# Performance work log

Measured on AMD Instinct MI355X. Metric: run time of the kernel, lower is better.

The kernel has to match this reference:

```python
import jax, jax.numpy as jnp
import numpy as np

N, C = 262144, 512
EPS = 1e-7


def setup_inputs() -> dict:
    key = jax.random.key(0)
    k1, k2, k3 = jax.random.split(key, 3)
    close_er = jax.random.normal(k1, (N, C), dtype=jnp.float32)
    y = jax.random.randint(k2, (N,), 0, C, dtype=jnp.int64)
    max_dis = jax.random.normal(k3, (C,), dtype=jnp.float32)
    margin = jnp.float32(0.5)
    return {"close_er": close_er, "y": y, "max_dis": max_dis, "margin": margin}


def reference(close_er, y, max_dis, margin):
    # Original: for each class i, take samples with y==i, compute
    # -log(clamp(sigmoid(close_er[idx, i] - max_dis[i] - margin))).mean(),
    # then average over classes that have at least one sample.
    num_classes = max_dis.shape[0]
    # Per-sample gather of its own-class distance: close_er[n, y[n]]
    ce = jnp.take_along_axis(close_er, y[:, None], axis=1)[:, 0]  # [N]
    md = max_dis[y]  # [N]
    gap = jax.nn.sigmoid(ce - md - margin)
    gap = jnp.clip(gap, EPS, 1.0 - EPS)
    nll = -jnp.log(gap)  # [N]
    # Per-class sum and count in one segment-reduce pass over N.
    sums = jax.ops.segment_sum(nll, y, num_segments=num_classes)  # [C]
    counts = jax.ops.segment_sum(jnp.ones_like(nll), y, num_segments=num_classes)  # [C]
    nonempty = counts > 0
    means = jnp.where(nonempty, sums / jnp.maximum(counts, 1.0), 0.0)
    j = jnp.sum(nonempty).astype(means.dtype)
    return jnp.sum(means) / j
```

## Files before the change

kernel.cpp:

```cpp
#include <hip/hip_runtime.h>

#define N_CLASSES 512
#define EPS_F 1e-7f

__global__ __launch_bounds__(1024) void nll_hist_kernel(
    const float* __restrict__ close_er,
    const int*   __restrict__ y,
    const float* __restrict__ max_dis,
    const float* __restrict__ margin_p,
    float* __restrict__ g_sums,
    float* __restrict__ g_counts,
    int n)
{
    __shared__ float        s_md[N_CLASSES];
    __shared__ float        s_sum[N_CLASSES];
    __shared__ unsigned int s_cnt[N_CLASSES];

    const int tid = threadIdx.x;
    const float margin = margin_p[0];

    for (int c = tid; c < N_CLASSES; c += blockDim.x) {
        s_md[c]  = max_dis[c];
        s_sum[c] = 0.0f;
        s_cnt[c] = 0u;
    }
    __syncthreads();

    for (long long i = (long long)blockIdx.x * blockDim.x + tid; i < n;
         i += (long long)gridDim.x * blockDim.x) {
        const int c = y[i];
        const float ce = close_er[i * (long long)N_CLASSES + c];
        const float x  = ce - s_md[c] - margin;
        float s = 1.0f / (1.0f + __expf(-x));
        s = fminf(fmaxf(s, EPS_F), 1.0f - EPS_F);
        const float nll = -__logf(s);
        atomicAdd(&s_sum[c], nll);
        atomicAdd(&s_cnt[c], 1u);
    }
    __syncthreads();

    for (int c = tid; c < N_CLASSES; c += blockDim.x) {
        const unsigned int cnt = s_cnt[c];
        if (cnt != 0u) {
            atomicAdd(&g_sums[c],   s_sum[c]);
            atomicAdd(&g_counts[c], (float)cnt);
        }
    }
}

__global__ __launch_bounds__(512) void finalize_kernel(
    const float* __restrict__ g_sums,
    const float* __restrict__ g_counts,
    float* __restrict__ out)
{
    __shared__ float s_m[N_CLASSES];
    __shared__ float s_j[N_CLASSES];

    const int t = threadIdx.x;
    const float cnt  = g_counts[t];
    const bool  ne   = cnt > 0.0f;
    s_m[t] = ne ? (g_sums[t] / cnt) : 0.0f;
    s_j[t] = ne ? 1.0f : 0.0f;
    __syncthreads();

    for (int off = 256; off >= 64; off >>= 1) {
        if (t < off) {
            s_m[t] += s_m[t + off];
            s_j[t] += s_j[t + off];
        }
        __syncthreads();
    }
    if (t < 64) {
        float m = s_m[t];
        float j = s_j[t];
        for (int off = 32; off > 0; off >>= 1) {
            m += __shfl_down(m, off);
            j += __shfl_down(j, off);
        }
        if (t == 0) out[0] = m / j;
    }
}

extern "C" void kernel_launch(void* const* d_in, const int* in_sizes, int n_in,
                              void* d_out, int out_size, void* d_ws, size_t ws_size,
                              hipStream_t stream) {
    const float* close_er = (const float*)d_in[0];
    const int*   y        = (const int*)d_in[1];
    const float* max_dis  = (const float*)d_in[2];
    const float* margin   = (const float*)d_in[3];
    float* out = (float*)d_out;

    const int n = in_sizes[1];

    float* g_sums   = (float*)d_ws;
    float* g_counts = g_sums + N_CLASSES;

    hipMemsetAsync(d_ws, 0, 2 * N_CLASSES * sizeof(float), stream);

    const int block = 1024;
    const int grid  = (n + block - 1) / block;
    nll_hist_kernel<<<grid, block, 0, stream>>>(close_er, y, max_dis, margin,
                                                g_sums, g_counts, n);
    finalize_kernel<<<1, N_CLASSES, 0, stream>>>(g_sums, g_counts, out);
}
```

Before: 21.70 us.

## Fuse finalize into histogram kernel via last-block ticket and batch four samples per thread

```diff
diff --git a/kernel.cpp b/kernel.cpp
--- a/kernel.cpp
+++ b/kernel.cpp
@@ -2,82 +2,122 @@
 
 #define N_CLASSES 512
 #define EPS_F 1e-7f
+#define BLOCK 256
+#define SPT 4
 
-__global__ __launch_bounds__(1024) void nll_hist_kernel(
+__global__ __launch_bounds__(BLOCK) void nll_fused_kernel(
     const float* __restrict__ close_er,
     const int*   __restrict__ y,
     const float* __restrict__ max_dis,
     const float* __restrict__ margin_p,
     float* __restrict__ g_sums,
     float* __restrict__ g_counts,
+    int*   __restrict__ g_ticket,
+    float* __restrict__ out,
     int n)
 {
     __shared__ float        s_md[N_CLASSES];
     __shared__ float        s_sum[N_CLASSES];
     __shared__ unsigned int s_cnt[N_CLASSES];
+    __shared__ float        s_red[8];
+    __shared__ bool         s_last;
 
     const int tid = threadIdx.x;
     const float margin = margin_p[0];
 
-    for (int c = tid; c < N_CLASSES; c += blockDim.x) {
+    for (int c = tid; c < N_CLASSES; c += BLOCK) {
         s_md[c]  = max_dis[c];
         s_sum[c] = 0.0f;
         s_cnt[c] = 0u;
     }
     __syncthreads();
 
-    for (long long i = (long long)blockIdx.x * blockDim.x + tid; i < n;
-         i += (long long)gridDim.x * blockDim.x) {
-        const int c = y[i];
-        const float ce = close_er[i * (long long)N_CLASSES + c];
-        const float x  = ce - s_md[c] - margin;
-        float s = 1.0f / (1.0f + __expf(-x));
-        s = fminf(fmaxf(s, EPS_F), 1.0f - EPS_F);
-        const float nll = -__logf(s);
-        atomicAdd(&s_sum[c], nll);
-        atomicAdd(&s_cnt[c], 1u);
+    const int base = (blockIdx.x * BLOCK + tid) * SPT;
+    if (base + SPT <= n) {
+        const int4 y4 = *reinterpret_cast<const int4*>(&y[base]);
+        const int c0 = y4.x, c1 = y4.y, c2 = y4.z, c3 = y4.w;
+        const float ce0 = close_er[(size_t)(base + 0) * N_CLASSES + c0];
+        const float ce1 = close_er[(size_t)(base + 1) * N_CLASSES + c1];
+        const float ce2 = close_er[(size_t)(base + 2) * N_CLASSES + c2];
+        const float ce3 = close_er[(size_t)(base + 3) * N_CLASSES + c3];
+        const float x0 = ce0 - s_md[c0] - margin;
+        const float x1 = ce1 - s_md[c1] - margin;
+        const float x2 = ce2 - s_md[c2] - margin;
+        const float x3 = ce3 - s_md[c3] - margin;
+        float s0 = 1.0f / (1.0f + __expf(-x0));
+        float s1 = 1.0f / (1.0f + __expf(-x1));
+        float s2 = 1.0f / (1.0f + __expf(-x2));
+        float s3 = 1.0f / (1.0f + __expf(-x3));
+        s0 = fminf(fmaxf(s0, EPS_F), 1.0f - EPS_F);
+        s1 = fminf(fmaxf(s1, EPS_F), 1.0f - EPS_F);
+        s2 = fminf(fmaxf(s2, EPS_F), 1.0f - EPS_F);
+        s3 = fminf(fmaxf(s3, EPS_F), 1.0f - EPS_F);
+        atomicAdd(&s_sum[c0], -__logf(s0));
+        atomicAdd(&s_sum[c1], -__logf(s1));
+        atomicAdd(&s_sum[c2], -__logf(s2));
+        atomicAdd(&s_sum[c3], -__logf(s3));
+        atomicAdd(&s_cnt[c0], 1u);
+        atomicAdd(&s_cnt[c1], 1u);
+        atomicAdd(&s_cnt[c2], 1u);
+        atomicAdd(&s_cnt[c3], 1u);
+    } else {
+        for (int k = 0; k < SPT; ++k) {
+            const int i = base + k;
+            if (i < n) {
+                const int c = y[i];
+                const float ce = close_er[(size_t)i * N_CLASSES + c];
+                const float x  = ce - s_md[c] - margin;
+                float s = 1.0f / (1.0f + __expf(-x));
+                s = fminf(fmaxf(s, EPS_F), 1.0f - EPS_F);
+                atomicAdd(&s_sum[c], -__logf(s));
+                atomicAdd(&s_cnt[c], 1u);
+            }
+        }
     }
     __syncthreads();
 
-    for (int c = tid; c < N_CLASSES; c += blockDim.x) {
+    for (int c = tid; c < N_CLASSES; c += BLOCK) {
         const unsigned int cnt = s_cnt[c];
         if (cnt != 0u) {
             atomicAdd(&g_sums[c],   s_sum[c]);
             atomicAdd(&g_counts[c], (float)cnt);
         }
     }
-}
 
-__global__ __launch_bounds__(512) void finalize_kernel(
-    const float* __restrict__ g_sums,
-    const float* __restrict__ g_counts,
-    float* __restrict__ out)
-{
-    __shared__ float s_m[N_CLASSES];
-    __shared__ float s_j[N_CLASSES];
+    __threadfence();
+    if (tid == 0) {
+        const int t = atomicAdd(g_ticket, 1);
+        s_last = (t == (int)gridDim.x - 1);
+    }
+    __syncthreads();
+    if (!s_last) return;
+    __threadfence();
 
-    const int t = threadIdx.x;
-    const float cnt  = g_counts[t];
-    const bool  ne   = cnt > 0.0f;
-    s_m[t] = ne ? (g_sums[t] / cnt) : 0.0f;
-    s_j[t] = ne ? 1.0f : 0.0f;
+    float m = 0.0f, j = 0.0f;
+    for (int c = tid; c < N_CLASSES; c += BLOCK) {
+        const float cnt = g_counts[c];
+        if (cnt > 0.0f) {
+            m += g_sums[c] / cnt;
+            j += 1.0f;
+        }
+    }
+    for (int off = 32; off > 0; off >>= 1) {
+        m += __shfl_down(m, off);
+        j += __shfl_down(j, off);
+    }
+    const int wave = tid >> 6;
+    if ((tid & 63) == 0) {
+        s_red[wave * 2]     = m;
+        s_red[wave * 2 + 1] = j;
+    }
     __syncthreads();
-
-    for (int off = 256; off >= 64; off >>= 1) {
-        if (t < off) {
-            s_m[t] += s_m[t + off];
-            s_j[t] += s_j[t + off];
+    if (tid == 0) {
+        float M = 0.0f, J = 0.0f;
+        for (int w = 0; w < BLOCK / 64; ++w) {
+            M += s_red[w * 2];
+            J += s_red[w * 2 + 1];
         }
-        __syncthreads();
-    }
-    if (t < 64) {
-        float m = s_m[t];
-        float j = s_j[t];
-        for (int off = 32; off > 0; off >>= 1) {
-            m += __shfl_down(m, off);
-            j += __shfl_down(j, off);
-        }
-        if (t == 0) out[0] = m / j;
+        out[0] = M / J;
     }
 }
 
@@ -94,12 +134,12 @@
 
     float* g_sums   = (float*)d_ws;
     float* g_counts = g_sums + N_CLASSES;
+    int*   g_ticket = (int*)(g_counts + N_CLASSES);
 
-    hipMemsetAsync(d_ws, 0, 2 * N_CLASSES * sizeof(float), stream);
+    hipMemsetAsync(d_ws, 0, (2 * N_CLASSES + 1) * sizeof(float), stream);
 
-    const int block = 1024;
-    const int grid  = (n + block - 1) / block;
-    nll_hist_kernel<<<grid, block, 0, stream>>>(close_er, y, max_dis, margin,
-                                                g_sums, g_counts, n);
-    finalize_kernel<<<1, N_CLASSES, 0, stream>>>(g_sums, g_counts, out);
+    const int grid = (n + BLOCK * SPT - 1) / (BLOCK * SPT);
+    nll_fused_kernel<<<grid, BLOCK, 0, stream>>>(close_er, y, max_dis, margin,
+                                                 g_sums, g_counts, g_ticket,
+                                                 out, n);
 }
```

Measured after the change: 34.41 us. +58.5%, slower.
